# Performance work log

Hardware: AMD Instinct MI355X
Metric: run time of the kernel (lower is better)

## Reference

```python
import jax, jax.numpy as jnp
import numpy as np

N = 50000      # nodes
E = 800000     # edges (avg degree 16)
IN = 128       # in_channels
OUT = 64       # out_channels
K = 2          # propagation hops


def setup_inputs() -> dict:
    key = jax.random.key(0)
    k1, k2, k3 = jax.random.split(key, 3)
    x = jax.random.normal(k1, (N, IN), dtype=jnp.float32)
    edge_index = jax.random.randint(k2, (2, E), 0, N, dtype=jnp.int32)
    # SGConv's internal Linear(in, out): weight [OUT, IN], bias [OUT]
    W = jax.random.normal(k3, (OUT, IN), dtype=jnp.float32) / np.sqrt(IN)
    b = jnp.zeros((OUT,), dtype=jnp.float32)
    return {"x": x, "edge_index": edge_index, "W": W, "b": b}


def reference(x, edge_index, W, b):
    # GCN normalization with self-loops (PyG gcn_norm, add_self_loops=True)
    row, col = edge_index[0], edge_index[1]
    loops = jnp.arange(N, dtype=edge_index.dtype)
    row = jnp.concatenate([row, loops])   # source nodes
    col = jnp.concatenate([col, loops])   # target nodes
    ones = jnp.ones((E + N,), dtype=x.dtype)
    deg = jax.ops.segment_sum(ones, col, num_segments=N)          # in-degree incl. self-loop
    deg_inv_sqrt = jnp.where(deg > 0, jax.lax.rsqrt(deg), 0.0)
    norm = deg_inv_sqrt[row] * deg_inv_sqrt[col]                  # [E+N]

    # K-hop propagation: x <- D^{-1/2} (A+I) D^{-1/2} x
    for _ in range(K):
        x = jax.ops.segment_sum(x[row] * norm[:, None], col, num_segments=N)

    # final linear; dropout is identity in eval mode (training=False)
    return x @ W.T + b
```

## Files before the change

kernel.cpp:

```cpp
#include <hip/hip_runtime.h>
#include <hip/hip_bf16.h>
#include <hip/hip_fp16.h>

#define IN_CH 128
#define OUT_CH 64
#define NB 512

typedef _Float16 hh2 __attribute__((ext_vector_type(2)));

__global__ void __launch_bounds__(512) histo_kernel(const int* __restrict__ col,
                                                    int* __restrict__ blkcnt,
                                                    int E, int chunk) {
    __shared__ int h[256];
    int blk = blockIdx.x, tid = threadIdx.x;
    if (tid < 256) h[tid] = 0;
    __syncthreads();
    int s = blk * chunk, e = min(s + chunk, E);
    for (int i = s + tid; i < e; i += 512)
        atomicAdd(&h[col[i] >> 8], 1);
    __syncthreads();
    if (tid < 256) blkcnt[blk * 256 + tid] = h[tid];
}

__global__ void __launch_bounds__(256) scanblk_kernel(int* __restrict__ blkcnt,
                                                      int* __restrict__ totals) {
    __shared__ int ps[256];
    int b = blockIdx.x, tid = threadIdx.x;
    int i0 = (2 * tid) * 256 + b, i1 = (2 * tid + 1) * 256 + b;
    int a0 = blkcnt[i0], a1 = blkcnt[i1];
    int lsum = a0 + a1;
    ps[tid] = lsum;
    __syncthreads();
    for (int d = 1; d < 256; d <<= 1) {
        int t = 0;
        if (tid >= d) t = ps[tid - d];
        __syncthreads();
        if (tid >= d) ps[tid] += t;
        __syncthreads();
    }
    int excl = ps[tid] - lsum;
    blkcnt[i0] = excl;
    blkcnt[i1] = excl + a0;
    if (tid == 255) totals[b] = excl + lsum;
}

__global__ void __launch_bounds__(512) bucket_scatter_kernel(const int* __restrict__ row,
                                                             const int* __restrict__ col,
                                                             const int* __restrict__ blkcnt,
                                                             const int* __restrict__ totals,
                                                             unsigned int* __restrict__ tmp,
                                                             int E, int chunk, int nbkt) {
    __shared__ int ps[256];
    __shared__ int cur[256];
    int blk = blockIdx.x, tid = threadIdx.x;
    int v = 0;
    if (tid < 256) { v = (tid < nbkt) ? totals[tid] : 0; ps[tid] = v; }
    __syncthreads();
    for (int d = 1; d < 256; d <<= 1) {
        int t = 0;
        if (tid < 256 && tid >= d) t = ps[tid - d];
        __syncthreads();
        if (tid < 256 && tid >= d) ps[tid] += t;
        __syncthreads();
    }
    if (tid < 256) cur[tid] = (ps[tid] - v) + blkcnt[blk * 256 + tid];
    __syncthreads();
    int s = blk * chunk, e = min(s + chunk, E);
    for (int i = s + tid; i < e; i += 512) {
        int c = col[i], r = row[i];
        int p = atomicAdd(&cur[c >> 8], 1);
        tmp[p] = ((unsigned)(c & 255) << 16) | (unsigned)r;
    }
}

__global__ void __launch_bounds__(512) bucket_sort_kernel(const unsigned int* __restrict__ tmp,
                                                          const int* __restrict__ totals,
                                                          int* __restrict__ off,
                                                          float* __restrict__ dis,
                                                          unsigned short* __restrict__ eidx,
                                                          int nbkt, int E, int n) {
    __shared__ int bs[256];
    __shared__ int cntl[256];
    __shared__ int sc[256];
    __shared__ int posl[256];
    int b = blockIdx.x, tid = threadIdx.x;
    int v = 0;
    if (tid < 256) { v = (tid < nbkt) ? totals[tid] : 0; bs[tid] = v; }
    __syncthreads();
    for (int d = 1; d < 256; d <<= 1) {
        int t = 0;
        if (tid < 256 && tid >= d) t = bs[tid - d];
        __syncthreads();
        if (tid < 256 && tid >= d) bs[tid] += t;
        __syncthreads();
    }
    if (tid < 256) bs[tid] -= v;
    if (tid < 256) cntl[tid] = 0;
    __syncthreads();
    int s = bs[b];
    int e = s + ((b < nbkt) ? totals[b] : 0);
    for (int i = s + tid; i < e; i += 512)
        atomicAdd(&cntl[tmp[i] >> 16], 1);
    __syncthreads();
    int c = 0;
    if (tid < 256) { c = cntl[tid]; sc[tid] = c; }
    __syncthreads();
    for (int d = 1; d < 256; d <<= 1) {
        int t = 0;
        if (tid < 256 && tid >= d) t = sc[tid - d];
        __syncthreads();
        if (tid < 256 && tid >= d) sc[tid] += t;
        __syncthreads();
    }
    if (tid < 256) {
        int excl = sc[tid] - c;
        int gid = (b << 8) + tid;
        if (gid < n) {
            off[gid] = s + excl;
            dis[gid] = rsqrtf((float)(c + 1));
        }
        posl[tid] = s + excl;
    }
    if (b == 0 && tid == 0) off[n] = E;
    __syncthreads();
    for (int i = s + tid; i < e; i += 512) {
        unsigned int w = tmp[i];
        int p = atomicAdd(&posl[w >> 16], 1);
        eidx[p] = (unsigned short)(w & 0xFFFFu);
    }
}

__global__ void __launch_bounds__(256) gemm_kernel(const float* __restrict__ x,
                                                   const float* __restrict__ W,
                                                   const float* __restrict__ dis,
                                                   __half* __restrict__ z, int n) {
    __shared__ hh2 Xs[64 * 66];
    __shared__ hh2 Ws[64 * 66];
    int t = threadIdx.x;
    int m0 = blockIdx.x * 64;
#pragma unroll
    for (int r = 0; r < 8; ++r) {
        int f = t + 256 * r;
        int o = f >> 5, kq = f & 31;
        float4 w = ((const float4*)W)[f];
        Ws[o * 66 + kq * 2]     = hh2{(_Float16)w.x, (_Float16)w.y};
        Ws[o * 66 + kq * 2 + 1] = hh2{(_Float16)w.z, (_Float16)w.w};
    }
#pragma unroll
    for (int r = 0; r < 8; ++r) {
        int f = t + 256 * r;
        int node = f >> 5, kq = f & 31;
        int gv = min(m0 + node, n - 1);
        float4 xv = ((const float4*)(x + (size_t)gv * IN_CH))[kq];
        Xs[node * 66 + kq * 2]     = hh2{(_Float16)xv.x, (_Float16)xv.y};
        Xs[node * 66 + kq * 2 + 1] = hh2{(_Float16)xv.z, (_Float16)xv.w};
    }
    __syncthreads();
    int tx = t & 15, ty = t >> 4;
    float acc[4][4];
#pragma unroll
    for (int i = 0; i < 4; ++i)
#pragma unroll
        for (int j = 0; j < 4; ++j) acc[i][j] = 0.f;

#pragma unroll 4
    for (int kq = 0; kq < 32; ++kq) {
        hh2 xa0[4], xa1[4], wb0[4], wb1[4];
#pragma unroll
        for (int i = 0; i < 4; ++i) {
            int base = (tx + 16 * i) * 66 + kq * 2;
            xa0[i] = Xs[base]; xa1[i] = Xs[base + 1];
        }
#pragma unroll
        for (int j = 0; j < 4; ++j) {
            int base = (ty * 4 + j) * 66 + kq * 2;
            wb0[j] = Ws[base]; wb1[j] = Ws[base + 1];
        }
#pragma unroll
        for (int i = 0; i < 4; ++i)
#pragma unroll
            for (int j = 0; j < 4; ++j) {
                float s = acc[i][j];
                s = __builtin_amdgcn_fdot2(xa0[i], wb0[j], s, false);
                s = __builtin_amdgcn_fdot2(xa1[i], wb1[j], s, false);
                acc[i][j] = s;
            }
    }
#pragma unroll
    for (int i = 0; i < 4; ++i) {
        int v = m0 + tx + 16 * i;
        if (v < n) {
            float dv = dis[v];
            union { __half2 h[2]; float2 f; } u;
            u.h[0] = __floats2half2_rn(dv * acc[i][0], dv * acc[i][1]);
            u.h[1] = __floats2half2_rn(dv * acc[i][2], dv * acc[i][3]);
            *(float2*)&z[(size_t)v * OUT_CH + ty * 4] = u.f;
        }
    }
}

template <int MODE>
__global__ void __launch_bounds__(256) hop_kernel(const __half* __restrict__ zin,
                                                  void* __restrict__ out,
                                                  const unsigned short* __restrict__ eidx,
                                                  const int* __restrict__ off,
                                                  const float* __restrict__ dis,
                                                  const float* __restrict__ bias, int n) {
    int v = (int)((blockIdx.x * 256 + threadIdx.x) >> 6);
    if (v >= n) return;
    int lane = threadIdx.x & 63;
    int grp = lane >> 3;
    int sub = lane & 7;
    int s = off[v], e = off[v + 1];
    float a0 = 0.f, a1 = 0.f, a2 = 0.f, a3 = 0.f;
    float a4 = 0.f, a5 = 0.f, a6 = 0.f, a7 = 0.f;
    if (grp == 0) {
        float4 raw = ((const float4*)(zin + (size_t)v * OUT_CH))[sub];
        const __half2* h2 = (const __half2*)&raw;
        float2 f0 = __half22float2(h2[0]), f1 = __half22float2(h2[1]);
        float2 f2 = __half22float2(h2[2]), f3 = __half22float2(h2[3]);
        a0 = f0.x; a1 = f0.y; a2 = f1.x; a3 = f1.y;
        a4 = f2.x; a5 = f2.y; a6 = f3.x; a7 = f3.y;
    }
    int i0 = s + grp, i1 = s + grp + 8;
    bool h0 = i0 < e, h1 = i1 < e;
    int r0 = h0 ? (int)eidx[i0] : 0;
    int r1 = h1 ? (int)eidx[i1] : 0;
    while (h0) {
        int j0 = i0 + 16, j1 = i1 + 16;
        bool g0 = j0 < e, g1 = j1 < e;
        int q0 = g0 ? (int)eidx[j0] : 0;
        int q1 = g1 ? (int)eidx[j1] : 0;
        float4 rawA = make_float4(0.f, 0.f, 0.f, 0.f);
        float4 rawB = make_float4(0.f, 0.f, 0.f, 0.f);
        if (h0) rawA = ((const float4*)(zin + (size_t)r0 * OUT_CH))[sub];
        if (h1) rawB = ((const float4*)(zin + (size_t)r1 * OUT_CH))[sub];
        {
            const __half2* hA = (const __half2*)&rawA;
            float2 f0 = __half22float2(hA[0]), f1 = __half22float2(hA[1]);
            float2 f2 = __half22float2(hA[2]), f3 = __half22float2(hA[3]);
            a0 += f0.x; a1 += f0.y; a2 += f1.x; a3 += f1.y;
            a4 += f2.x; a5 += f2.y; a6 += f3.x; a7 += f3.y;
        }
        {
            const __half2* hB = (const __half2*)&rawB;
            float2 f0 = __half22float2(hB[0]), f1 = __half22float2(hB[1]);
            float2 f2 = __half22float2(hB[2]), f3 = __half22float2(hB[3]);
            a0 += f0.x; a1 += f0.y; a2 += f1.x; a3 += f1.y;
            a4 += f2.x; a5 += f2.y; a6 += f3.x; a7 += f3.y;
        }
        i0 = j0; i1 = j1; r0 = q0; r1 = q1; h0 = g0; h1 = g1;
    }
#pragma unroll
    for (int m = 8; m <= 32; m <<= 1) {
        a0 += __shfl_xor(a0, m, 64); a1 += __shfl_xor(a1, m, 64);
        a2 += __shfl_xor(a2, m, 64); a3 += __shfl_xor(a3, m, 64);
        a4 += __shfl_xor(a4, m, 64); a5 += __shfl_xor(a5, m, 64);
        a6 += __shfl_xor(a6, m, 64); a7 += __shfl_xor(a7, m, 64);
    }
    if (grp == 0) {
        float dv = dis[v];
        if (MODE == 0) {
            float sc = dv * dv;
            union { __half2 h[4]; float4 f; } u;
            u.h[0] = __floats2half2_rn(sc * a0, sc * a1);
            u.h[1] = __floats2half2_rn(sc * a2, sc * a3);
            u.h[2] = __floats2half2_rn(sc * a4, sc * a5);
            u.h[3] = __floats2half2_rn(sc * a6, sc * a7);
            ((float4*)((__half*)out + (size_t)v * OUT_CH))[sub] = u.f;
        } else {
            const float4* bp = (const float4*)(bias + sub * 8);
            float4 b0 = bp[0], b1 = bp[1];
            float* op = (float*)out + (size_t)v * OUT_CH + sub * 8;
            *(float4*)op = make_float4(fmaf(dv, a0, b0.x), fmaf(dv, a1, b0.y),
                                       fmaf(dv, a2, b0.z), fmaf(dv, a3, b0.w));
            *(float4*)(op + 4) = make_float4(fmaf(dv, a4, b1.x), fmaf(dv, a5, b1.y),
                                             fmaf(dv, a6, b1.z), fmaf(dv, a7, b1.w));
        }
    }
}

extern "C" void kernel_launch(void* const* d_in, const int* in_sizes, int n_in,
                              void* d_out, int out_size, void* d_ws, size_t ws_size,
                              hipStream_t stream) {
    const float* x = (const float*)d_in[0];
    const int* ei = (const int*)d_in[1];
    const float* W = (const float*)d_in[2];
    const float* b = (const float*)d_in[3];
    int n = in_sizes[0] / IN_CH;
    int E = in_sizes[1] / 2;
    const int* row = ei;
    const int* col = ei + E;

    char* ws = (char*)d_ws;
    size_t o = 0;
    auto alloc = [&](size_t bytes) -> void* {
        void* p = ws + o;
        o += (bytes + 255) & ~(size_t)255;
        return p;
    };
    int nbkt = (n + 255) >> 8;
    int chunk = (E + NB - 1) / NB;

    int*            blkcnt = (int*)alloc((size_t)NB * 256 * 4);
    int*            totals = (int*)alloc(256 * 4);
    unsigned int*   tmp    = (unsigned int*)alloc((size_t)E * 4);
    int*            off    = (int*)alloc((size_t)(n + 1) * 4);
    float*          dis    = (float*)alloc((size_t)n * 4);
    unsigned short* eidx   = (unsigned short*)alloc((size_t)E * 2);
    __half*         zA     = (__half*)alloc((size_t)n * OUT_CH * 2);
    __half*         zB     = (__half*)alloc((size_t)n * OUT_CH * 2);

    histo_kernel<<<NB, 512, 0, stream>>>(col, blkcnt, E, chunk);
    scanblk_kernel<<<nbkt, 256, 0, stream>>>(blkcnt, totals);
    bucket_scatter_kernel<<<NB, 512, 0, stream>>>(row, col, blkcnt, totals, tmp, E, chunk, nbkt);
    bucket_sort_kernel<<<nbkt, 512, 0, stream>>>(tmp, totals, off, dis, eidx, nbkt, E, n);
    gemm_kernel<<<(n + 63) / 64, 256, 0, stream>>>(x, W, dis, zA, n);
    int hopBlocks = (n + 3) / 4;
    hop_kernel<0><<<hopBlocks, 256, 0, stream>>>(zA, zB, eidx, off, dis, nullptr, n);
    hop_kernel<1><<<hopBlocks, 256, 0, stream>>>(zB, d_out, eidx, off, dis, b, n);
}
```

Before: 159.9 us.

## Fuse all seven stages into one cooperative persistent kernel with grid syncs

Replaces the seven separate launches (histogram, scan, scatter, bucket sort, GEMM, two propagation hops) with a single cooperative kernel of 512 blocks × 256 threads that separates the stages with grid.sync(). GEMM tiles and hop node-groups are now looped over persistently, and shared memory is reused across phases. This removes per-launch overhead and inter-kernel gaps. In exchange the whole grid must wait at each barrier, and the hop phases get far fewer resident blocks than before to hide gather latency.

```diff
diff --git a/kernel.cpp b/kernel.cpp
--- a/kernel.cpp
+++ b/kernel.cpp
@@ -1,296 +1,303 @@
 #include <hip/hip_runtime.h>
 #include <hip/hip_bf16.h>
 #include <hip/hip_fp16.h>
+#include <hip/hip_cooperative_groups.h>
+
+namespace cg = cooperative_groups;
 
 #define IN_CH 128
 #define OUT_CH 64
-#define NB 512
+#define NBLK 512
+#define NTHR 256
 
 typedef _Float16 hh2 __attribute__((ext_vector_type(2)));
 
-__global__ void __launch_bounds__(512) histo_kernel(const int* __restrict__ col,
-                                                    int* __restrict__ blkcnt,
-                                                    int E, int chunk) {
-    __shared__ int h[256];
+template <int MODE>
+__device__ __forceinline__ void hop_phase(const __half* __restrict__ zin,
+                                          void* __restrict__ out,
+                                          const unsigned short* __restrict__ eidx,
+                                          const int* __restrict__ off,
+                                          const float* __restrict__ dis,
+                                          const float* __restrict__ bias,
+                                          int n, int blk, int tid) {
+    int lane = tid & 63;
+    int wavei = tid >> 6;
+    int grp = lane >> 3;
+    int sub = lane & 7;
+    int nGroups = (n + 3) >> 2;
+    for (int gq = blk; gq < nGroups; gq += NBLK) {
+        int v = gq * 4 + wavei;
+        if (v >= n) continue;
+        int s = off[v], e = off[v + 1];
+        float a0 = 0.f, a1 = 0.f, a2 = 0.f, a3 = 0.f;
+        float a4 = 0.f, a5 = 0.f, a6 = 0.f, a7 = 0.f;
+        if (grp == 0) {
+            float4 raw = ((const float4*)(zin + (size_t)v * OUT_CH))[sub];
+            const __half2* h2 = (const __half2*)&raw;
+            float2 f0 = __half22float2(h2[0]), f1 = __half22float2(h2[1]);
+            float2 f2 = __half22float2(h2[2]), f3 = __half22float2(h2[3]);
+            a0 = f0.x; a1 = f0.y; a2 = f1.x; a3 = f1.y;
+            a4 = f2.x; a5 = f2.y; a6 = f3.x; a7 = f3.y;
+        }
+        int i0 = s + grp, i1 = s + grp + 8;
+        bool h0 = i0 < e, h1 = i1 < e;
+        int r0 = h0 ? (int)eidx[i0] : 0;
+        int r1 = h1 ? (int)eidx[i1] : 0;
+        while (h0) {
+            int j0 = i0 + 16, j1 = i1 + 16;
+            bool g0 = j0 < e, g1 = j1 < e;
+            int q0 = g0 ? (int)eidx[j0] : 0;
+            int q1 = g1 ? (int)eidx[j1] : 0;
+            float4 rawA = make_float4(0.f, 0.f, 0.f, 0.f);
+            float4 rawB = make_float4(0.f, 0.f, 0.f, 0.f);
+            if (h0) rawA = ((const float4*)(zin + (size_t)r0 * OUT_CH))[sub];
+            if (h1) rawB = ((const float4*)(zin + (size_t)r1 * OUT_CH))[sub];
+            {
+                const __half2* hA = (const __half2*)&rawA;
+                float2 f0 = __half22float2(hA[0]), f1 = __half22float2(hA[1]);
+                float2 f2 = __half22float2(hA[2]), f3 = __half22float2(hA[3]);
+                a0 += f0.x; a1 += f0.y; a2 += f1.x; a3 += f1.y;
+                a4 += f2.x; a5 += f2.y; a6 += f3.x; a7 += f3.y;
+            }
+            {
+                const __half2* hB = (const __half2*)&rawB;
+                float2 f0 = __half22float2(hB[0]), f1 = __half22float2(hB[1]);
+                float2 f2 = __half22float2(hB[2]), f3 = __half22float2(hB[3]);
+                a0 += f0.x; a1 += f0.y; a2 += f1.x; a3 += f1.y;
+                a4 += f2.x; a5 += f2.y; a6 += f3.x; a7 += f3.y;
+            }
+            i0 = j0; i1 = j1; r0 = q0; r1 = q1; h0 = g0; h1 = g1;
+        }
+#pragma unroll
+        for (int m = 8; m <= 32; m <<= 1) {
+            a0 += __shfl_xor(a0, m, 64); a1 += __shfl_xor(a1, m, 64);
+            a2 += __shfl_xor(a2, m, 64); a3 += __shfl_xor(a3, m, 64);
+            a4 += __shfl_xor(a4, m, 64); a5 += __shfl_xor(a5, m, 64);
+            a6 += __shfl_xor(a6, m, 64); a7 += __shfl_xor(a7, m, 64);
+        }
+        if (grp == 0) {
+            float dv = dis[v];
+            if (MODE == 0) {
+                float sc = dv * dv;
+                union { __half2 h[4]; float4 f; } u;
+                u.h[0] = __floats2half2_rn(sc * a0, sc * a1);
+                u.h[1] = __floats2half2_rn(sc * a2, sc * a3);
+                u.h[2] = __floats2half2_rn(sc * a4, sc * a5);
+                u.h[3] = __floats2half2_rn(sc * a6, sc * a7);
+                ((float4*)((__half*)out + (size_t)v * OUT_CH))[sub] = u.f;
+            } else {
+                const float4* bp = (const float4*)(bias + sub * 8);
+                float4 b0 = bp[0], b1 = bp[1];
+                float* op = (float*)out + (size_t)v * OUT_CH + sub * 8;
+                *(float4*)op = make_float4(fmaf(dv, a0, b0.x), fmaf(dv, a1, b0.y),
+                                           fmaf(dv, a2, b0.z), fmaf(dv, a3, b0.w));
+                *(float4*)(op + 4) = make_float4(fmaf(dv, a4, b1.x), fmaf(dv, a5, b1.y),
+                                                 fmaf(dv, a6, b1.z), fmaf(dv, a7, b1.w));
+            }
+        }
+    }
+}
+
+__global__ void __launch_bounds__(NTHR, 2) mega_kernel(
+    const int* __restrict__ row, const int* __restrict__ col,
+    const float* __restrict__ x, const float* __restrict__ W,
+    const float* __restrict__ bias,
+    int* __restrict__ blkcnt, int* __restrict__ totals,
+    unsigned int* __restrict__ tmp, int* __restrict__ off,
+    float* __restrict__ dis, unsigned short* __restrict__ eidx,
+    __half* __restrict__ zA, __half* __restrict__ zB,
+    float* __restrict__ out, int E, int n, int nbkt, int chunk) {
+    cg::grid_group grid = cg::this_grid();
+    __shared__ __align__(16) char smem[2 * 64 * 66 * sizeof(hh2)];
     int blk = blockIdx.x, tid = threadIdx.x;
-    if (tid < 256) h[tid] = 0;
-    __syncthreads();
-    int s = blk * chunk, e = min(s + chunk, E);
-    for (int i = s + tid; i < e; i += 512)
-        atomicAdd(&h[col[i] >> 8], 1);
-    __syncthreads();
-    if (tid < 256) blkcnt[blk * 256 + tid] = h[tid];
-}
-
-__global__ void __launch_bounds__(256) scanblk_kernel(int* __restrict__ blkcnt,
-                                                      int* __restrict__ totals) {
-    __shared__ int ps[256];
-    int b = blockIdx.x, tid = threadIdx.x;
-    int i0 = (2 * tid) * 256 + b, i1 = (2 * tid + 1) * 256 + b;
-    int a0 = blkcnt[i0], a1 = blkcnt[i1];
-    int lsum = a0 + a1;
-    ps[tid] = lsum;
-    __syncthreads();
-    for (int d = 1; d < 256; d <<= 1) {
-        int t = 0;
-        if (tid >= d) t = ps[tid - d];
-        __syncthreads();
-        if (tid >= d) ps[tid] += t;
-        __syncthreads();
-    }
-    int excl = ps[tid] - lsum;
-    blkcnt[i0] = excl;
-    blkcnt[i1] = excl + a0;
-    if (tid == 255) totals[b] = excl + lsum;
-}
-
-__global__ void __launch_bounds__(512) bucket_scatter_kernel(const int* __restrict__ row,
-                                                             const int* __restrict__ col,
-                                                             const int* __restrict__ blkcnt,
-                                                             const int* __restrict__ totals,
-                                                             unsigned int* __restrict__ tmp,
-                                                             int E, int chunk, int nbkt) {
-    __shared__ int ps[256];
-    __shared__ int cur[256];
-    int blk = blockIdx.x, tid = threadIdx.x;
-    int v = 0;
-    if (tid < 256) { v = (tid < nbkt) ? totals[tid] : 0; ps[tid] = v; }
-    __syncthreads();
-    for (int d = 1; d < 256; d <<= 1) {
-        int t = 0;
-        if (tid < 256 && tid >= d) t = ps[tid - d];
-        __syncthreads();
-        if (tid < 256 && tid >= d) ps[tid] += t;
-        __syncthreads();
-    }
-    if (tid < 256) cur[tid] = (ps[tid] - v) + blkcnt[blk * 256 + tid];
-    __syncthreads();
-    int s = blk * chunk, e = min(s + chunk, E);
-    for (int i = s + tid; i < e; i += 512) {
-        int c = col[i], r = row[i];
-        int p = atomicAdd(&cur[c >> 8], 1);
-        tmp[p] = ((unsigned)(c & 255) << 16) | (unsigned)r;
-    }
-}
-
-__global__ void __launch_bounds__(512) bucket_sort_kernel(const unsigned int* __restrict__ tmp,
-                                                          const int* __restrict__ totals,
-                                                          int* __restrict__ off,
-                                                          float* __restrict__ dis,
-                                                          unsigned short* __restrict__ eidx,
-                                                          int nbkt, int E, int n) {
-    __shared__ int bs[256];
-    __shared__ int cntl[256];
-    __shared__ int sc[256];
-    __shared__ int posl[256];
-    int b = blockIdx.x, tid = threadIdx.x;
-    int v = 0;
-    if (tid < 256) { v = (tid < nbkt) ? totals[tid] : 0; bs[tid] = v; }
-    __syncthreads();
-    for (int d = 1; d < 256; d <<= 1) {
-        int t = 0;
-        if (tid < 256 && tid >= d) t = bs[tid - d];
-        __syncthreads();
-        if (tid < 256 && tid >= d) bs[tid] += t;
-        __syncthreads();
-    }
-    if (tid < 256) bs[tid] -= v;
-    if (tid < 256) cntl[tid] = 0;
-    __syncthreads();
-    int s = bs[b];
-    int e = s + ((b < nbkt) ? totals[b] : 0);
-    for (int i = s + tid; i < e; i += 512)
-        atomicAdd(&cntl[tmp[i] >> 16], 1);
-    __syncthreads();
-    int c = 0;
-    if (tid < 256) { c = cntl[tid]; sc[tid] = c; }
-    __syncthreads();
-    for (int d = 1; d < 256; d <<= 1) {
-        int t = 0;
-        if (tid < 256 && tid >= d) t = sc[tid - d];
-        __syncthreads();
-        if (tid < 256 && tid >= d) sc[tid] += t;
-        __syncthreads();
-    }
-    if (tid < 256) {
+
+    {
+        int* h = (int*)smem;
+        h[tid] = 0;
+        __syncthreads();
+        int s = blk * chunk, e = min(s + chunk, E);
+        for (int i = s + tid; i < e; i += NTHR)
+            atomicAdd(&h[col[i] >> 8], 1);
+        __syncthreads();
+        blkcnt[blk * 256 + tid] = h[tid];
+    }
+    grid.sync();
+
+    if (blk < nbkt) {
+        int* ps = (int*)smem;
+        int i0 = (2 * tid) * 256 + blk, i1 = (2 * tid + 1) * 256 + blk;
+        int a0 = blkcnt[i0], a1 = blkcnt[i1];
+        int lsum = a0 + a1;
+        ps[tid] = lsum;
+        __syncthreads();
+        for (int d = 1; d < 256; d <<= 1) {
+            int t2 = 0;
+            if (tid >= d) t2 = ps[tid - d];
+            __syncthreads();
+            if (tid >= d) ps[tid] += t2;
+            __syncthreads();
+        }
+        int excl = ps[tid] - lsum;
+        blkcnt[i0] = excl;
+        blkcnt[i1] = excl + a0;
+        if (tid == 255) totals[blk] = excl + lsum;
+    }
+    grid.sync();
+
+    {
+        int* ps = (int*)smem;
+        int* cur = ps + 256;
+        int v = (tid < nbkt) ? totals[tid] : 0;
+        ps[tid] = v;
+        __syncthreads();
+        for (int d = 1; d < 256; d <<= 1) {
+            int t2 = 0;
+            if (tid >= d) t2 = ps[tid - d];
+            __syncthreads();
+            if (tid >= d) ps[tid] += t2;
+            __syncthreads();
+        }
+        cur[tid] = (ps[tid] - v) + blkcnt[blk * 256 + tid];
+        __syncthreads();
+        int s = blk * chunk, e = min(s + chunk, E);
+        for (int i = s + tid; i < e; i += NTHR) {
+            int c = col[i], r = row[i];
+            int p = atomicAdd(&cur[c >> 8], 1);
+            tmp[p] = ((unsigned)(c & 255) << 16) | (unsigned)r;
+        }
+    }
+    grid.sync();
+
+    if (blk < nbkt) {
+        int* bs = (int*)smem;
+        int* cntl = bs + 256;
+        int* sc = cntl + 256;
+        int* posl = sc + 256;
+        int v = (tid < nbkt) ? totals[tid] : 0;
+        bs[tid] = v;
+        __syncthreads();
+        for (int d = 1; d < 256; d <<= 1) {
+            int t2 = 0;
+            if (tid >= d) t2 = bs[tid - d];
+            __syncthreads();
+            if (tid >= d) bs[tid] += t2;
+            __syncthreads();
+        }
+        bs[tid] -= v;
+        cntl[tid] = 0;
+        __syncthreads();
+        int s = bs[blk], e = s + totals[blk];
+        for (int i = s + tid; i < e; i += NTHR)
+            atomicAdd(&cntl[tmp[i] >> 16], 1);
+        __syncthreads();
+        int c = cntl[tid];
+        sc[tid] = c;
+        __syncthreads();
+        for (int d = 1; d < 256; d <<= 1) {
+            int t2 = 0;
+            if (tid >= d) t2 = sc[tid - d];
+            __syncthreads();
+            if (tid >= d) sc[tid] += t2;
+            __syncthreads();
+        }
         int excl = sc[tid] - c;
-        int gid = (b << 8) + tid;
+        int gid = (blk << 8) + tid;
         if (gid < n) {
             off[gid] = s + excl;
             dis[gid] = rsqrtf((float)(c + 1));
         }
         posl[tid] = s + excl;
-    }
-    if (b == 0 && tid == 0) off[n] = E;
-    __syncthreads();
-    for (int i = s + tid; i < e; i += 512) {
-        unsigned int w = tmp[i];
-        int p = atomicAdd(&posl[w >> 16], 1);
-        eidx[p] = (unsigned short)(w & 0xFFFFu);
-    }
-}
-
-__global__ void __launch_bounds__(256) gemm_kernel(const float* __restrict__ x,
-                                                   const float* __restrict__ W,
-                                                   const float* __restrict__ dis,
-                                                   __half* __restrict__ z, int n) {
-    __shared__ hh2 Xs[64 * 66];
-    __shared__ hh2 Ws[64 * 66];
-    int t = threadIdx.x;
-    int m0 = blockIdx.x * 64;
-#pragma unroll
-    for (int r = 0; r < 8; ++r) {
-        int f = t + 256 * r;
-        int o = f >> 5, kq = f & 31;
-        float4 w = ((const float4*)W)[f];
-        Ws[o * 66 + kq * 2]     = hh2{(_Float16)w.x, (_Float16)w.y};
-        Ws[o * 66 + kq * 2 + 1] = hh2{(_Float16)w.z, (_Float16)w.w};
-    }
-#pragma unroll
-    for (int r = 0; r < 8; ++r) {
-        int f = t + 256 * r;
-        int node = f >> 5, kq = f & 31;
-        int gv = min(m0 + node, n - 1);
-        float4 xv = ((const float4*)(x + (size_t)gv * IN_CH))[kq];
-        Xs[node * 66 + kq * 2]     = hh2{(_Float16)xv.x, (_Float16)xv.y};
-        Xs[node * 66 + kq * 2 + 1] = hh2{(_Float16)xv.z, (_Float16)xv.w};
-    }
-    __syncthreads();
-    int tx = t & 15, ty = t >> 4;
-    float acc[4][4];
-#pragma unroll
-    for (int i = 0; i < 4; ++i)
-#pragma unroll
-        for (int j = 0; j < 4; ++j) acc[i][j] = 0.f;
-
+        if (blk == 0 && tid == 0) off[n] = E;
+        __syncthreads();
+        for (int i = s + tid; i < e; i += NTHR) {
+            unsigned int w = tmp[i];
+            int p = atomicAdd(&posl[w >> 16], 1);
+            eidx[p] = (unsigned short)(w & 0xFFFFu);
+        }
+    }
+    grid.sync();
+
+    {
+        hh2* Xs = (hh2*)smem;
+        hh2* Ws = (hh2*)(smem + 64 * 66 * sizeof(hh2));
+#pragma unroll
+        for (int r = 0; r < 8; ++r) {
+            int f = tid + NTHR * r;
+            int o = f >> 5, kq = f & 31;
+            float4 w = ((const float4*)W)[f];
+            Ws[o * 66 + kq * 2]     = hh2{(_Float16)w.x, (_Float16)w.y};
+            Ws[o * 66 + kq * 2 + 1] = hh2{(_Float16)w.z, (_Float16)w.w};
+        }
+        int nTiles = (n + 63) >> 6;
+        int tx = tid & 15, ty = tid >> 4;
+        for (int tile = blk; tile < nTiles; tile += NBLK) {
+            __syncthreads();
+            int m0 = tile * 64;
+#pragma unroll
+            for (int r = 0; r < 8; ++r) {
+                int f = tid + NTHR * r;
+                int node = f >> 5, kq = f & 31;
+                int gv = min(m0 + node, n - 1);
+                float4 xv = ((const float4*)(x + (size_t)gv * IN_CH))[kq];
+                Xs[node * 66 + kq * 2]     = hh2{(_Float16)xv.x, (_Float16)xv.y};
+                Xs[node * 66 + kq * 2 + 1] = hh2{(_Float16)xv.z, (_Float16)xv.w};
+            }
+            __syncthreads();
+            float acc[4][4];
+#pragma unroll
+            for (int i = 0; i < 4; ++i)
+#pragma unroll
+                for (int j = 0; j < 4; ++j) acc[i][j] = 0.f;
 #pragma unroll 4
-    for (int kq = 0; kq < 32; ++kq) {
-        hh2 xa0[4], xa1[4], wb0[4], wb1[4];
-#pragma unroll
-        for (int i = 0; i < 4; ++i) {
-            int base = (tx + 16 * i) * 66 + kq * 2;
-            xa0[i] = Xs[base]; xa1[i] = Xs[base + 1];
-        }
-#pragma unroll
-        for (int j = 0; j < 4; ++j) {
-            int base = (ty * 4 + j) * 66 + kq * 2;
-            wb0[j] = Ws[base]; wb1[j] = Ws[base + 1];
-        }
-#pragma unroll
-        for (int i = 0; i < 4; ++i)
-#pragma unroll
-            for (int j = 0; j < 4; ++j) {
-                float s = acc[i][j];
-                s = __builtin_amdgcn_fdot2(xa0[i], wb0[j], s, false);
-                s = __builtin_amdgcn_fdot2(xa1[i], wb1[j], s, false);
-                acc[i][j] = s;
-            }
-    }
-#pragma unroll
-    for (int i = 0; i < 4; ++i) {
-        int v = m0 + tx + 16 * i;
-        if (v < n) {
-            float dv = dis[v];
-            union { __half2 h[2]; float2 f; } u;
-            u.h[0] = __floats2half2_rn(dv * acc[i][0], dv * acc[i][1]);
-            u.h[1] = __floats2half2_rn(dv * acc[i][2], dv * acc[i][3]);
-            *(float2*)&z[(size_t)v * OUT_CH + ty * 4] = u.f;
-        }
-    }
-}
-
-template <int MODE>
-__global__ void __launch_bounds__(256) hop_kernel(const __half* __restrict__ zin,
-                                                  void* __restrict__ out,
-                                                  const unsigned short* __restrict__ eidx,
-                                                  const int* __restrict__ off,
-                                                  const float* __restrict__ dis,
-                                                  const float* __restrict__ bias, int n) {
-    int v = (int)((blockIdx.x * 256 + threadIdx.x) >> 6);
-    if (v >= n) return;
-    int lane = threadIdx.x & 63;
-    int grp = lane >> 3;
-    int sub = lane & 7;
-    int s = off[v], e = off[v + 1];
-    float a0 = 0.f, a1 = 0.f, a2 = 0.f, a3 = 0.f;
-    float a4 = 0.f, a5 = 0.f, a6 = 0.f, a7 = 0.f;
-    if (grp == 0) {
-        float4 raw = ((const float4*)(zin + (size_t)v * OUT_CH))[sub];
-        const __half2* h2 = (const __half2*)&raw;
-        float2 f0 = __half22float2(h2[0]), f1 = __half22float2(h2[1]);
-        float2 f2 = __half22float2(h2[2]), f3 = __half22float2(h2[3]);
-        a0 = f0.x; a1 = f0.y; a2 = f1.x; a3 = f1.y;
-        a4 = f2.x; a5 = f2.y; a6 = f3.x; a7 = f3.y;
-    }
-    int i0 = s + grp, i1 = s + grp + 8;
-    bool h0 = i0 < e, h1 = i1 < e;
-    int r0 = h0 ? (int)eidx[i0] : 0;
-    int r1 = h1 ? (int)eidx[i1] : 0;
-    while (h0) {
-        int j0 = i0 + 16, j1 = i1 + 16;
-        bool g0 = j0 < e, g1 = j1 < e;
-        int q0 = g0 ? (int)eidx[j0] : 0;
-        int q1 = g1 ? (int)eidx[j1] : 0;
-        float4 rawA = make_float4(0.f, 0.f, 0.f, 0.f);
-        float4 rawB = make_float4(0.f, 0.f, 0.f, 0.f);
-        if (h0) rawA = ((const float4*)(zin + (size_t)r0 * OUT_CH))[sub];
-        if (h1) rawB = ((const float4*)(zin + (size_t)r1 * OUT_CH))[sub];
-        {
-            const __half2* hA = (const __half2*)&rawA;
-            float2 f0 = __half22float2(hA[0]), f1 = __half22float2(hA[1]);
-            float2 f2 = __half22float2(hA[2]), f3 = __half22float2(hA[3]);
-            a0 += f0.x; a1 += f0.y; a2 += f1.x; a3 += f1.y;
-            a4 += f2.x; a5 += f2.y; a6 += f3.x; a7 += f3.y;
-        }
-        {
-            const __half2* hB = (const __half2*)&rawB;
-            float2 f0 = __half22float2(hB[0]), f1 = __half22float2(hB[1]);
-            float2 f2 = __half22float2(hB[2]), f3 = __half22float2(hB[3]);
-            a0 += f0.x; a1 += f0.y; a2 += f1.x; a3 += f1.y;
-            a4 += f2.x; a5 += f2.y; a6 += f3.x; a7 += f3.y;
-        }
-        i0 = j0; i1 = j1; r0 = q0; r1 = q1; h0 = g0; h1 = g1;
-    }
-#pragma unroll
-    for (int m = 8; m <= 32; m <<= 1) {
-        a0 += __shfl_xor(a0, m, 64); a1 += __shfl_xor(a1, m, 64);
-        a2 += __shfl_xor(a2, m, 64); a3 += __shfl_xor(a3, m, 64);
-        a4 += __shfl_xor(a4, m, 64); a5 += __shfl_xor(a5, m, 64);
-        a6 += __shfl_xor(a6, m, 64); a7 += __shfl_xor(a7, m, 64);
-    }
-    if (grp == 0) {
-        float dv = dis[v];
-        if (MODE == 0) {
-            float sc = dv * dv;
-            union { __half2 h[4]; float4 f; } u;
-            u.h[0] = __floats2half2_rn(sc * a0, sc * a1);
-            u.h[1] = __floats2half2_rn(sc * a2, sc * a3);
-            u.h[2] = __floats2half2_rn(sc * a4, sc * a5);
-            u.h[3] = __floats2half2_rn(sc * a6, sc * a7);
-            ((float4*)((__half*)out + (size_t)v * OUT_CH))[sub] = u.f;
-        } else {
-            const float4* bp = (const float4*)(bias + sub * 8);
-            float4 b0 = bp[0], b1 = bp[1];
-            float* op = (float*)out + (size_t)v * OUT_CH + sub * 8;
-            *(float4*)op = make_float4(fmaf(dv, a0, b0.x), fmaf(dv, a1, b0.y),
-                                       fmaf(dv, a2, b0.z), fmaf(dv, a3, b0.w));
-            *(float4*)(op + 4) = make_float4(fmaf(dv, a4, b1.x), fmaf(dv, a5, b1.y),
-                                             fmaf(dv, a6, b1.z), fmaf(dv, a7, b1.w));
-        }
-    }
+            for (int kq = 0; kq < 32; ++kq) {
+                hh2 xa0[4], xa1[4], wb0[4], wb1[4];
+#pragma unroll
+                for (int i = 0; i < 4; ++i) {
+                    int base = (tx + 16 * i) * 66 + kq * 2;
+                    xa0[i] = Xs[base]; xa1[i] = Xs[base + 1];
+                }
+#pragma unroll
+                for (int j = 0; j < 4; ++j) {
+                    int base = (ty * 4 + j) * 66 + kq * 2;
+                    wb0[j] = Ws[base]; wb1[j] = Ws[base + 1];
+                }
+#pragma unroll
+                for (int i = 0; i < 4; ++i)
+#pragma unroll
+                    for (int j = 0; j < 4; ++j) {
+                        float s = acc[i][j];
+                        s = __builtin_amdgcn_fdot2(xa0[i], wb0[j], s, false);
+                        s = __builtin_amdgcn_fdot2(xa1[i], wb1[j], s, false);
+                        acc[i][j] = s;
+                    }
+            }
+#pragma unroll
+            for (int i = 0; i < 4; ++i) {
+                int v = m0 + tx + 16 * i;
+                if (v < n) {
+                    float dv = dis[v];
+                    union { __half2 h[2]; float2 f; } u;
+                    u.h[0] = __floats2half2_rn(dv * acc[i][0], dv * acc[i][1]);
+                    u.h[1] = __floats2half2_rn(dv * acc[i][2], dv * acc[i][3]);
+                    *(float2*)&zA[(size_t)v * OUT_CH + ty * 4] = u.f;
+                }
+            }
+        }
+    }
+    grid.sync();
+
+    hop_phase<0>(zA, zB, eidx, off, dis, nullptr, n, blk, tid);
+    grid.sync();
+
+    hop_phase<1>(zB, out, eidx, off, dis, bias, n, blk, tid);
 }
 
 extern "C" void kernel_launch(void* const* d_in, const int* in_sizes, int n_in,
                               void* d_out, int out_size, void* d_ws, size_t ws_size,
                               hipStream_t stream) {
-    const float* x = (const float*)d_in[0];
     const int* ei = (const int*)d_in[1];
-    const float* W = (const float*)d_in[2];
-    const float* b = (const float*)d_in[3];
     int n = in_sizes[0] / IN_CH;
     int E = in_sizes[1] / 2;
-    const int* row = ei;
-    const int* col = ei + E;
 
     char* ws = (char*)d_ws;
     size_t o = 0;
@@ -300,9 +307,9 @@
         return p;
     };
     int nbkt = (n + 255) >> 8;
-    int chunk = (E + NB - 1) / NB;
-
-    int*            blkcnt = (int*)alloc((size_t)NB * 256 * 4);
+    int chunk = (E + NBLK - 1) / NBLK;
+
+    int*            blkcnt = (int*)alloc((size_t)NBLK * 256 * 4);
     int*            totals = (int*)alloc(256 * 4);
     unsigned int*   tmp    = (unsigned int*)alloc((size_t)E * 4);
     int*            off    = (int*)alloc((size_t)(n + 1) * 4);
@@ -311,12 +318,19 @@
     __half*         zA     = (__half*)alloc((size_t)n * OUT_CH * 2);
     __half*         zB     = (__half*)alloc((size_t)n * OUT_CH * 2);
 
-    histo_kernel<<<NB, 512, 0, stream>>>(col, blkcnt, E, chunk);
-    scanblk_kernel<<<nbkt, 256, 0, stream>>>(blkcnt, totals);
-    bucket_scatter_kernel<<<NB, 512, 0, stream>>>(row, col, blkcnt, totals, tmp, E, chunk, nbkt);
-    bucket_sort_kernel<<<nbkt, 512, 0, stream>>>(tmp, totals, off, dis, eidx, nbkt, E, n);
-    gemm_kernel<<<(n + 63) / 64, 256, 0, stream>>>(x, W, dis, zA, n);
-    int hopBlocks = (n + 3) / 4;
-    hop_kernel<0><<<hopBlocks, 256, 0, stream>>>(zA, zB, eidx, off, dis, nullptr, n);
-    hop_kernel<1><<<hopBlocks, 256, 0, stream>>>(zB, d_out, eidx, off, dis, b, n);
+    const int*   row_  = ei;
+    const int*   col_  = ei + E;
+    const float* x_    = (const float*)d_in[0];
+    const float* W_    = (const float*)d_in[2];
+    const float* b_    = (const float*)d_in[3];
+    float*       out_  = (float*)d_out;
+
+    void* kargs[] = {
+        (void*)&row_, (void*)&col_, (void*)&x_, (void*)&W_, (void*)&b_,
+        (void*)&blkcnt, (void*)&totals, (void*)&tmp, (void*)&off,
+        (void*)&dis, (void*)&eidx, (void*)&zA, (void*)&zB,
+        (void*)&out_, (void*)&E, (void*)&n, (void*)&nbkt, (void*)&chunk
+    };
+    hipLaunchCooperativeKernel((const void*)mega_kernel, dim3(NBLK), dim3(NTHR),
+                               kargs, 0, stream);
 }
```

Result: slower. 573.8 us (+258.9%).
